# Kernel optimization log

Hardware: AMD Instinct MI355X
Metric: run time of the kernel (lower is better)

The kernel has to match this reference:

```python
import math
import jax, jax.numpy as jnp
import numpy as np

B, L, D_MODEL, NHEAD, FACTOR = 8, 4096, 1024, 16, 5
D_HEAD = D_MODEL // NHEAD
SAMPLE_K = min(L, max(1, FACTOR * int(math.ceil(math.log(max(L, 2))))))  # 45
TOP_U = min(L, max(1, FACTOR * int(math.ceil(math.log(max(L, 2))))))     # 45


def setup_inputs() -> dict:
    key = jax.random.key(0)
    ks = jax.random.split(key, 10)
    x = jax.random.normal(ks[0], (B, L, D_MODEL), dtype=jnp.float32)
    sample_idx = jax.random.randint(ks[1], (SAMPLE_K,), 0, L)
    s = 0.02
    Wq = jax.random.normal(ks[2], (D_MODEL, D_MODEL), dtype=jnp.float32) * s
    Wk = jax.random.normal(ks[3], (D_MODEL, D_MODEL), dtype=jnp.float32) * s
    Wv = jax.random.normal(ks[4], (D_MODEL, D_MODEL), dtype=jnp.float32) * s
    Wo = jax.random.normal(ks[5], (D_MODEL, D_MODEL), dtype=jnp.float32) * s
    bq = jnp.zeros((D_MODEL,), dtype=jnp.float32)
    bk = jnp.zeros((D_MODEL,), dtype=jnp.float32)
    bv = jnp.zeros((D_MODEL,), dtype=jnp.float32)
    bo = jnp.zeros((D_MODEL,), dtype=jnp.float32)
    return {"x": x, "Wq": Wq, "bq": bq, "Wk": Wk, "bk": bk, "Wv": Wv, "bv": bv, "Wo": Wo, "bo": bo, "sample_idx": sample_idx}


def _split_heads(t):
    b, l, _ = t.shape
    return t.reshape(b, l, NHEAD, D_HEAD).transpose(0, 2, 1, 3)  # (b, h, l, d)


def reference(x, Wq, bq, Wk, bk, Wv, bv, Wo, bo, sample_idx):
    b, l, d = x.shape
    q = _split_heads(x @ Wq.T + bq)  # (b, h, l, dh)
    k = _split_heads(x @ Wk.T + bk)
    v = _split_heads(x @ Wv.T + bv)
    scale = 1.0 / math.sqrt(D_HEAD)

    # sparsity measurement on sampled keys
    k_sample = k[:, :, sample_idx, :]                          # (b, h, S, dh)
    scores_sample = jnp.einsum('bhqd,bhsd->bhqs', q, k_sample) * scale
    m = scores_sample.max(axis=-1) - scores_sample.mean(axis=-1)  # (b, h, l)
    _, top_idx = jax.lax.top_k(m, TOP_U)                       # (b, h, U)

    # mean-of-values initialization for non-selected queries
    context = jnp.broadcast_to(v.mean(axis=-2, keepdims=True), (b, NHEAD, l, D_HEAD))

    # dense attention only for the top-U queries
    q_top = jnp.take_along_axis(q, top_idx[..., None], axis=2)  # (b, h, U, dh)
    scores_top = jnp.einsum('bhud,bhkd->bhuk', q_top, k) * scale
    attn = jax.nn.softmax(scores_top, axis=-1)
    out_top = jnp.einsum('bhuk,bhkd->bhud', attn, v)            # (b, h, U, dh)

    bi = jnp.arange(b)[:, None, None]
    hi = jnp.arange(NHEAD)[None, :, None]
    context = context.at[bi, hi, top_idx].set(out_top)          # scatter back

    out = context.transpose(0, 2, 1, 3).reshape(b, l, d)
    return out @ Wo.T + bo
```

## Files before the change

kernel.cpp:

```cpp
#include <hip/hip_runtime.h>
#include <cfloat>
#include <cstdint>

#define B_  8
#define L_  4096
#define DM  1024
#define NH  16
#define DH  64
#define SK  45

typedef __attribute__((ext_vector_type(4))) float f32x4;
typedef _Float16 f16;
typedef __attribute__((ext_vector_type(4))) _Float16 f16x4;
typedef __attribute__((ext_vector_type(8))) _Float16 f16x8;

__device__ __forceinline__ void gload_lds16(const void* g, void* l) {
  __builtin_amdgcn_global_load_lds(
      (const __attribute__((address_space(1))) unsigned int*)g,
      (__attribute__((address_space(3))) unsigned int*)l, 16, 0, 0);
}

__device__ __forceinline__ int swz(int row, int c) {
  return row * 32 + (c ^ (((row >> 1) & 3) << 3));
}

__global__ __launch_bounds__(256) void xsplit16_kernel(const float* __restrict__ x,
    f16* __restrict__ xh, int n4) {
  int i = blockIdx.x * 256 + threadIdx.x;
  int stride = gridDim.x * 256;
  for (; i < n4; i += stride) {
    f32x4 v = ((const f32x4*)x)[i];
    f16x4 h;
    #pragma unroll
    for (int j = 0; j < 4; ++j) h[j] = (f16)v[j];
    ((f16x4*)xh)[i] = h;
  }
}

__global__ __launch_bounds__(256) void wsplit16_kernel(const float* __restrict__ w,
    f16* __restrict__ wh, f16* __restrict__ wl, int n4, int withlo) {
  int i = blockIdx.x * 256 + threadIdx.x;
  int stride = gridDim.x * 256;
  for (; i < n4; i += stride) {
    f32x4 v = ((const f32x4*)w)[i];
    f16x4 h, l;
    #pragma unroll
    for (int j = 0; j < 4; ++j) {
      h[j] = (f16)v[j];
      l[j] = (f16)((v[j] - (float)h[j]) * 2048.0f);
    }
    ((f16x4*)wh)[i] = h;
    if (withlo) ((f16x4*)wl)[i] = l;
  }
}

__global__ __launch_bounds__(256) void meansum_kernel(const f16* __restrict__ xh,
                                                      float* __restrict__ meanx) {
  int b = blockIdx.x;
  int d = blockIdx.y * 256 + threadIdx.x;
  int l0 = blockIdx.z * 256;
  const f16* p = xh + ((size_t)b * L_ + l0) * DM + d;
  float s = 0.f;
  for (int i = 0; i < 256; ++i) s += (float)p[(size_t)i * DM];
  atomicAdd(&meanx[b * DM + d], s);
}

__global__ __launch_bounds__(256) void meansum32_kernel(const float* __restrict__ x,
                                                        float* __restrict__ meanx) {
  int b = blockIdx.x;
  int d = blockIdx.y * 256 + threadIdx.x;
  int l0 = blockIdx.z * 256;
  const float* p = x + ((size_t)b * L_ + l0) * DM + d;
  float s = 0.f;
  for (int i = 0; i < 256; ++i) s += p[(size_t)i * DM];
  atomicAdd(&meanx[b * DM + d], s);
}

__global__ __launch_bounds__(256) void proj_vec_kernel(const float* __restrict__ vin,
    const float* __restrict__ W, const float* __restrict__ bias,
    float* __restrict__ vout, float scale) {
  int g = blockIdx.x * 256 + threadIdx.x;
  int b = g >> 10, n = g & 1023;
  const float* xr = vin + b * DM;
  const float* wr = W + (size_t)n * DM;
  float a0 = 0, a1 = 0, a2 = 0, a3 = 0;
  for (int d = 0; d < DM; d += 4) {
    a0 += xr[d + 0] * wr[d + 0];
    a1 += xr[d + 1] * wr[d + 1];
    a2 += xr[d + 2] * wr[d + 2];
    a3 += xr[d + 3] * wr[d + 3];
  }
  vout[g] = ((a0 + a1) + (a2 + a3)) * scale + bias[n];
}

__global__ __launch_bounds__(256, 4) void ksample_kernel(const float* __restrict__ x,
    const float* __restrict__ Wk, const float* __restrict__ bk,
    const int* __restrict__ sidx, float* __restrict__ KS) {
  const int b = blockIdx.x, nc = blockIdx.y, sg = blockIdx.z;
  __shared__ float xs[5][32];
  __shared__ float wk[64][33];
  __shared__ float red[4][5][64];
  __shared__ int ls[5];
  const int tid = threadIdx.x;
  const int nl = tid & 63, kq = tid >> 6;
  if (tid < 5) ls[tid] = sidx[sg * 5 + tid];
  float acc[5] = {0.f, 0.f, 0.f, 0.f, 0.f};
  const int wrow = tid >> 2, wq = tid & 3;
  for (int kt = 0; kt < 32; ++kt) {
    const int d0 = kt * 32;
    __syncthreads();
    if (tid < 40) {
      int s = tid >> 3, q = tid & 7;
      *(f32x4*)&xs[s][q * 4] = *(const f32x4*)&x[((size_t)b * L_ + ls[s]) * DM + d0 + q * 4];
    }
    {
      const float* src = &Wk[(size_t)(nc * 64 + wrow) * DM + d0 + wq * 8];
      *(f32x4*)&wk[wrow][wq * 8]     = *(const f32x4*)src;
      *(f32x4*)&wk[wrow][wq * 8 + 4] = *(const f32x4*)(src + 4);
    }
    __syncthreads();
    #pragma unroll
    for (int i = 0; i < 2; ++i) {
      f32x4 w = *(const f32x4*)&wk[nl][kq * 8 + i * 4];
      #pragma unroll
      for (int s = 0; s < 5; ++s) {
        f32x4 xv = *(const f32x4*)&xs[s][kq * 8 + i * 4];
        acc[s] += xv[0] * w[0] + xv[1] * w[1] + xv[2] * w[2] + xv[3] * w[3];
      }
    }
  }
  #pragma unroll
  for (int s = 0; s < 5; ++s) red[kq][s][nl] = acc[s];
  __syncthreads();
  for (int t = tid; t < 5 * 64; t += 256) {
    int s = t >> 6, j = t & 63;
    int nj = nc * 64 + j;
    KS[((size_t)b * SK + sg * 5 + s) * DM + nj] =
        red[0][s][j] + red[1][s][j] + red[2][s][j] + red[3][s][j] + bk[nj];
  }
}

__global__ __launch_bounds__(256, 4) void pcomp_kernel(const float* __restrict__ Wq,
    const float* __restrict__ KS, f16* __restrict__ PH, f16* __restrict__ PL) {
  const int b = blockIdx.x, h = blockIdx.y, nc = blockIdx.z;
  __shared__ float ks[45][64];
  __shared__ float wqT[64][68];
  const int tid = threadIdx.x;
  const int n0 = nc * 64;
  for (int i = tid; i < 45 * 64; i += 256) {
    int s = i >> 6, d = i & 63;
    ks[s][d] = KS[((size_t)b * SK + s) * DM + h * 64 + d];
  }
  for (int t = tid; t < 1024; t += 256) {
    int row = t >> 4, cg = t & 15;
    f32x4 v = *(const f32x4*)&Wq[(size_t)(h * 64 + row) * DM + n0 + cg * 4];
    #pragma unroll
    for (int j = 0; j < 4; ++j) wqT[cg * 4 + j][row] = v[j];
  }
  __syncthreads();
  for (int t = tid; t < 48 * 64; t += 256) {
    int s = t >> 6, c = t & 63;
    float acc = 0.f;
    if (s < SK) {
      const f32x4* wr = (const f32x4*)&wqT[c][0];
      const f32x4* kr = (const f32x4*)&ks[s][0];
      float a0 = 0, a1 = 0, a2 = 0, a3 = 0;
      #pragma unroll
      for (int i = 0; i < 16; ++i) {
        f32x4 wv = wr[i], kv = kr[i];
        a0 += wv[0] * kv[0]; a1 += wv[1] * kv[1];
        a2 += wv[2] * kv[2]; a3 += wv[3] * kv[3];
      }
      acc = (a0 + a1) + (a2 + a3);
    }
    f16 hv = (f16)acc;
    size_t off = ((size_t)b * 768 + h * 48 + s) * DM + n0 + c;
    PH[off] = hv;
    PL[off] = (f16)((acc - (float)hv) * 2048.0f);
  }
}

__global__ __launch_bounds__(256, 2) void gemm_sc(const float* __restrict__ x,
    const f16* __restrict__ PH, const f16* __restrict__ PL,
    float* __restrict__ SC) {
  __shared__ f16 xh[128 * 32];
  __shared__ f16 xl[128 * 32];
  __shared__ f16 wh[128 * 32];
  __shared__ f16 wl[128 * 32];
  const int tid = threadIdx.x;
  const int g = blockIdx.y * 8 + blockIdx.x;
  const int q = g >> 3;
  const int nt = q % 6;
  const int mt = (g & 7) + (q / 6) * 8;
  const int n0 = nt * 128;
  const int m0 = mt * 128;
  const int bb = mt >> 5;
  const int lane = tid & 63;
  const int wave = tid >> 6;
  const int wr = (wave >> 1) * 64;
  const int wc = (wave & 1) * 64;
  const int frow = lane & 15;
  const int fk = (lane >> 4) * 8;

  f32x4 aH[4][4], aL[4][4];
  #pragma unroll
  for (int i = 0; i < 4; ++i)
    #pragma unroll
    for (int j = 0; j < 4; ++j)
      #pragma unroll
      for (int z = 0; z < 4; ++z) { aH[i][j][z] = 0.f; aL[i][j][z] = 0.f; }

  const int ar = tid >> 1;
  const int ac = (tid & 1) * 16;
  const int r2 = tid >> 2;
  const int cb = (tid & 3) * 8;
  const int cbs = cb ^ (((r2 >> 1) & 3) << 3);

  const size_t pbase = (size_t)bb * 768;
  for (int kt = 0; kt < 32; ++kt) {
    const float* gx = x + (size_t)(m0 + ar) * DM + kt * 32 + ac;
    #pragma unroll
    for (int gi = 0; gi < 4; ++gi) {
      f32x4 v = ((const f32x4*)gx)[gi];
      f16x4 h, l;
      #pragma unroll
      for (int z = 0; z < 4; ++z) {
        h[z] = (f16)v[z];
        l[z] = (f16)((v[z] - (float)h[z]) * 2048.0f);
      }
      *(f16x4*)(xh + swz(ar, ac + gi * 4)) = h;
      *(f16x4*)(xl + swz(ar, ac + gi * 4)) = l;
    }
    gload_lds16(PH + (pbase + n0 + r2) * DM + kt * 32 + cbs,      wh + r2 * 32 + cb);
    gload_lds16(PH + (pbase + n0 + r2 + 64) * DM + kt * 32 + cbs, wh + (r2 + 64) * 32 + cb);
    gload_lds16(PL + (pbase + n0 + r2) * DM + kt * 32 + cbs,      wl + r2 * 32 + cb);
    gload_lds16(PL + (pbase + n0 + r2 + 64) * DM + kt * 32 + cbs, wl + (r2 + 64) * 32 + cb);
    __syncthreads();
    f16x8 ah[4], al[4], bh[4], bl[4];
    #pragma unroll
    for (int mi = 0; mi < 4; ++mi) {
      ah[mi] = *(const f16x8*)(xh + swz(wr + mi * 16 + frow, fk));
      al[mi] = *(const f16x8*)(xl + swz(wr + mi * 16 + frow, fk));
    }
    #pragma unroll
    for (int ni = 0; ni < 4; ++ni) {
      bh[ni] = *(const f16x8*)(wh + swz(wc + ni * 16 + frow, fk));
      bl[ni] = *(const f16x8*)(wl + swz(wc + ni * 16 + frow, fk));
    }
    #pragma unroll
    for (int mi = 0; mi < 4; ++mi)
      #pragma unroll
      for (int ni = 0; ni < 4; ++ni) {
        aH[mi][ni] = __builtin_amdgcn_mfma_f32_16x16x32_f16(ah[mi], bh[ni], aH[mi][ni], 0, 0, 0);
        aL[mi][ni] = __builtin_amdgcn_mfma_f32_16x16x32_f16(ah[mi], bl[ni], aL[mi][ni], 0, 0, 0);
        aL[mi][ni] = __builtin_amdgcn_mfma_f32_16x16x32_f16(al[mi], bh[ni], aL[mi][ni], 0, 0, 0);
      }
    __syncthreads();
  }

  #pragma unroll
  for (int mi = 0; mi < 4; ++mi) {
    int rowb = m0 + wr + mi * 16 + (lane >> 4) * 4;
    #pragma unroll
    for (int ni = 0; ni < 4; ++ni) {
      int col = n0 + wc + ni * 16 + (lane & 15);
      #pragma unroll
      for (int j = 0; j < 4; ++j) {
        SC[(size_t)(rowb + j) * 768 + col] =
            (aH[mi][ni][j] + aL[mi][ni][j] * (1.0f / 2048.0f)) * 0.125f;
      }
    }
  }
}

__global__ __launch_bounds__(256) void mcompute_kernel(const float* __restrict__ SC,
    float* __restrict__ Mout) {
  const int b = blockIdx.x;
  const int l = blockIdx.y * 16 + (threadIdx.x >> 4);
  const int h = threadIdx.x & 15;
  const float* p = SC + ((size_t)(b * L_ + l)) * 768 + h * 48;
  float mx = -FLT_MAX, sum = 0.f;
  #pragma unroll
  for (int i = 0; i < 11; ++i) {
    f32x4 v = *(const f32x4*)(p + i * 4);
    #pragma unroll
    for (int j = 0; j < 4; ++j) { mx = fmaxf(mx, v[j]); sum += v[j]; }
  }
  { float v = p[44]; mx = fmaxf(mx, v); sum += v; }
  Mout[((size_t)(b * NH + h)) * L_ + l] = mx - sum * (1.0f / SK);
}

__global__ __launch_bounds__(256) void topk_kernel(const float* __restrict__ M,
                                                   int* __restrict__ topi) {
  __shared__ float vals[L_];
  __shared__ float wv[4];
  __shared__ int wi[4];
  const int bh = blockIdx.x, tid = threadIdx.x;
  for (int i = tid; i < L_; i += 256) vals[i] = M[(size_t)bh * L_ + i];
  __syncthreads();
  const int lane = tid & 63, wave = tid >> 6;
  for (int it = 0; it < SK; ++it) {
    float best = -FLT_MAX;
    int bi = 1 << 30;
    for (int i = tid; i < L_; i += 256) {
      float v = vals[i];
      if (v > best || (v == best && i < bi)) { best = v; bi = i; }
    }
    #pragma unroll
    for (int off = 32; off; off >>= 1) {
      float ov = __shfl_down(best, off);
      int oi = __shfl_down(bi, off);
      if (ov > best || (ov == best && oi < bi)) { best = ov; bi = oi; }
    }
    if (lane == 0) { wv[wave] = best; wi[wave] = bi; }
    __syncthreads();
    if (tid == 0) {
      float bb = wv[0]; int bj = wi[0];
      for (int w = 1; w < 4; ++w)
        if (wv[w] > bb || (wv[w] == bb && wi[w] < bj)) { bb = wv[w]; bj = wi[w]; }
      topi[bh * SK + it] = bj;
      vals[bj] = -FLT_MAX;
    }
    __syncthreads();
  }
}

__global__ __launch_bounds__(256, 4) void qtop5_kernel(const float* __restrict__ x,
    const float* __restrict__ Wq, const float* __restrict__ bq,
    const int* __restrict__ topi, f16* __restrict__ QT) {
  const int b = blockIdx.x, h = blockIdx.y, sg = blockIdx.z;
  const int bh = b * NH + h;
  __shared__ float xs[5][32];
  __shared__ float wq[64][33];
  __shared__ float red[4][5][64];
  __shared__ int ls[5];
  const int tid = threadIdx.x;
  const int nl = tid & 63, kq = tid >> 6;
  if (tid < 5) ls[tid] = topi[bh * SK + sg * 5 + tid];
  float acc[5] = {0.f, 0.f, 0.f, 0.f, 0.f};
  const int wrow = tid >> 2, wqc = tid & 3;
  for (int kt = 0; kt < 32; ++kt) {
    const int d0 = kt * 32;
    __syncthreads();
    if (tid < 40) {
      int s = tid >> 3, q = tid & 7;
      *(f32x4*)&xs[s][q * 4] = *(const f32x4*)&x[((size_t)b * L_ + ls[s]) * DM + d0 + q * 4];
    }
    {
      const float* src = &Wq[(size_t)(h * 64 + wrow) * DM + d0 + wqc * 8];
      *(f32x4*)&wq[wrow][wqc * 8]     = *(const f32x4*)src;
      *(f32x4*)&wq[wrow][wqc * 8 + 4] = *(const f32x4*)(src + 4);
    }
    __syncthreads();
    #pragma unroll
    for (int i = 0; i < 2; ++i) {
      f32x4 w = *(const f32x4*)&wq[nl][kq * 8 + i * 4];
      #pragma unroll
      for (int s = 0; s < 5; ++s) {
        f32x4 xv = *(const f32x4*)&xs[s][kq * 8 + i * 4];
        acc[s] += xv[0] * w[0] + xv[1] * w[1] + xv[2] * w[2] + xv[3] * w[3];
      }
    }
  }
  #pragma unroll
  for (int s = 0; s < 5; ++s) red[kq][s][nl] = acc[s];
  __syncthreads();
  for (int t = tid; t < 5 * 64; t += 256) {
    int s = t >> 6, j = t & 63;
    QT[bh * 3072 + (sg * 5 + s) * 64 + j] =
        (f16)(red[0][s][j] + red[1][s][j] + red[2][s][j] + red[3][s][j] + bq[h * 64 + j]);
  }
}

__global__ __launch_bounds__(256, 2) void kscore_kernel(const f16* __restrict__ XH,
    const f16* __restrict__ WKH, const f16* __restrict__ WVH,
    const float* __restrict__ bk, const float* __restrict__ bvec,
    const f16* __restrict__ QT, float* __restrict__ OT, float* __restrict__ Zb) {
  __shared__ __align__(16) char smem[68352];
  f16* qs = (f16*)smem;
  f16* xh = (f16*)(smem + 6912);
  f16* wh = (f16*)(smem + 23296);
  f16* Kt = (f16*)(smem + 31488);
  f16* Ps = (f16*)smem;
  f16* Vt = (f16*)(smem + 31488);
  float* red = (float*)smem;
  const int g = blockIdx.y * 128 + blockIdx.x;
  const int b = g & 7;
  const int p = g >> 3;
  const int jc = p >> 4;
  const int h = p & 15;
  const int bh = b * 16 + h;
  const int tid = threadIdx.x;
  const int lane = tid & 63, wave = tid >> 6;
  const int frow = lane & 15;
  const int fk = (lane >> 4) * 8;

  for (int i = tid; i < 48 * 64; i += 256)
    qs[(i >> 6) * 72 + (i & 63)] = QT[bh * 3072 + i];

  f32x4 accK[4][4], accV[4][4];
  #pragma unroll
  for (int i = 0; i < 4; ++i)
    #pragma unroll
    for (int j = 0; j < 4; ++j)
      #pragma unroll
      for (int z = 0; z < 4; ++z) { accK[i][j][z] = 0.f; accV[i][j][z] = 0.f; }

  const int r2 = tid >> 2, cb = (tid & 3) * 8;
  const int cbs = cb ^ (((r2 >> 1) & 3) << 3);
  for (int kt = 0; kt < 32; ++kt) {
    #pragma unroll
    for (int i = 0; i < 4; ++i)
      gload_lds16(XH + (size_t)(b * L_ + jc * 256 + i * 64 + r2) * DM + kt * 32 + cbs,
                  xh + (i * 64 + r2) * 32 + cb);
    gload_lds16(WKH + (size_t)(h * 64 + r2) * DM + kt * 32 + cbs, wh + r2 * 32 + cb);
    gload_lds16(WVH + (size_t)(h * 64 + r2) * DM + kt * 32 + cbs, wh + (r2 + 64) * 32 + cb);
    __syncthreads();
    f16x8 am[4], bnK[4], bnV[4];
    #pragma unroll
    for (int mi = 0; mi < 4; ++mi)
      am[mi] = *(const f16x8*)(xh + swz(wave * 64 + mi * 16 + frow, fk));
    #pragma unroll
    for (int ni = 0; ni < 4; ++ni) {
      bnK[ni] = *(const f16x8*)(wh + swz(ni * 16 + frow, fk));
      bnV[ni] = *(const f16x8*)(wh + swz(64 + ni * 16 + frow, fk));
    }
    #pragma unroll
    for (int mi = 0; mi < 4; ++mi)
      #pragma unroll
      for (int ni = 0; ni < 4; ++ni) {
        accK[mi][ni] = __builtin_amdgcn_mfma_f32_16x16x32_f16(am[mi], bnK[ni], accK[mi][ni], 0, 0, 0);
        accV[mi][ni] = __builtin_amdgcn_mfma_f32_16x16x32_f16(am[mi], bnV[ni], accV[mi][ni], 0, 0, 0);
      }
    __syncthreads();
  }

  #pragma unroll
  for (int mi = 0; mi < 4; ++mi) {
    int jl = wave * 64 + mi * 16 + (lane >> 4) * 4;
    #pragma unroll
    for (int ni = 0; ni < 4; ++ni) {
      int d = ni * 16 + (lane & 15);
      float bc = bk[h * 64 + d];
      #pragma unroll
      for (int z = 0; z < 4; ++z)
        Kt[(jl + z) * 72 + d] = (f16)(accK[mi][ni][z] + bc);
    }
  }
  __syncthreads();

  f32x4 accS[3][4];
  #pragma unroll
  for (int i = 0; i < 3; ++i)
    #pragma unroll
    for (int j = 0; j < 4; ++j)
      #pragma unroll
      for (int z = 0; z < 4; ++z) accS[i][j][z] = 0.f;
  #pragma unroll
  for (int ks = 0; ks < 2; ++ks) {
    f16x8 aq[3], bv[4];
    #pragma unroll
    for (int mu = 0; mu < 3; ++mu)
      aq[mu] = *(const f16x8*)(qs + (mu * 16 + frow) * 72 + ks * 32 + fk);
    #pragma unroll
    for (int nj = 0; nj < 4; ++nj)
      bv[nj] = *(const f16x8*)(Kt + (wave * 64 + nj * 16 + frow) * 72 + ks * 32 + fk);
    #pragma unroll
    for (int mu = 0; mu < 3; ++mu)
      #pragma unroll
      for (int nj = 0; nj < 4; ++nj)
        accS[mu][nj] = __builtin_amdgcn_mfma_f32_16x16x32_f16(aq[mu], bv[nj], accS[mu][nj], 0, 0, 0);
  }
  __syncthreads();

  #pragma unroll
  for (int mi = 0; mi < 4; ++mi) {
    int jl = wave * 64 + mi * 16 + (lane >> 4) * 4;
    #pragma unroll
    for (int ni = 0; ni < 4; ++ni) {
      int d = ni * 16 + (lane & 15);
      float bc = bvec[h * 64 + d];
      #pragma unroll
      for (int z = 0; z < 4; ++z)
        Vt[d * 264 + jl + z] = (f16)(accV[mi][ni][z] + bc);
    }
  }
  {
    float zs[3][4];
    #pragma unroll
    for (int mu = 0; mu < 3; ++mu)
      #pragma unroll
      for (int z = 0; z < 4; ++z) zs[mu][z] = 0.f;
    #pragma unroll
    for (int mu = 0; mu < 3; ++mu)
      #pragma unroll
      for (int nj = 0; nj < 4; ++nj) {
        int j = wave * 64 + nj * 16 + (lane & 15);
        #pragma unroll
        for (int z = 0; z < 4; ++z) {
          int u = mu * 16 + (lane >> 4) * 4 + z;
          float pv = __expf(accS[mu][nj][z] * 0.125f);
          Ps[u * 264 + j] = (f16)pv;
          zs[mu][z] += pv;
        }
      }
    #pragma unroll
    for (int mu = 0; mu < 3; ++mu)
      #pragma unroll
      for (int z = 0; z < 4; ++z) {
        float v = zs[mu][z];
        v += __shfl_xor(v, 1);
        v += __shfl_xor(v, 2);
        v += __shfl_xor(v, 4);
        v += __shfl_xor(v, 8);
        int u = mu * 16 + (lane >> 4) * 4 + z;
        if ((lane & 15) == 0 && u < SK) atomicAdd(&Zb[bh * 48 + u], v);
      }
  }
  __syncthreads();

  f32x4 accO[3][4];
  #pragma unroll
  for (int i = 0; i < 3; ++i)
    #pragma unroll
    for (int j = 0; j < 4; ++j)
      #pragma unroll
      for (int z = 0; z < 4; ++z) accO[i][j][z] = 0.f;
  #pragma unroll
  for (int ks = 0; ks < 2; ++ks) {
    f16x8 ap[3], bvv[4];
    #pragma unroll
    for (int mu = 0; mu < 3; ++mu)
      ap[mu] = *(const f16x8*)(Ps + (mu * 16 + frow) * 264 + wave * 64 + ks * 32 + fk);
    #pragma unroll
    for (int nd = 0; nd < 4; ++nd)
      bvv[nd] = *(const f16x8*)(Vt + (nd * 16 + frow) * 264 + wave * 64 + ks * 32 + fk);
    #pragma unroll
    for (int mu = 0; mu < 3; ++mu)
      #pragma unroll
      for (int nd = 0; nd < 4; ++nd)
        accO[mu][nd] = __builtin_amdgcn_mfma_f32_16x16x32_f16(ap[mu], bvv[nd], accO[mu][nd], 0, 0, 0);
  }
  __syncthreads();

  #pragma unroll
  for (int mu = 0; mu < 3; ++mu) {
    #pragma unroll
    for (int nd = 0; nd < 4; ++nd) {
      int d = nd * 16 + (lane & 15);
      #pragma unroll
      for (int z = 0; z < 4; ++z) {
        int u = mu * 16 + (lane >> 4) * 4 + z;
        red[wave * 3072 + u * 64 + d] = accO[mu][nd][z];
      }
    }
  }
  __syncthreads();
  for (int i = tid; i < 3072; i += 256) {
    int u = i >> 6;
    if (u < SK)
      atomicAdd(&OT[((size_t)bh * SK + u) * DH + (i & 63)],
                red[i] + red[3072 + i] + red[6144 + i] + red[9216 + i]);
  }
}

__global__ __launch_bounds__(256) void basewrite_kernel(const float* __restrict__ base,
                                                        float* __restrict__ out) {
  size_t i = (size_t)blockIdx.x * 256 + threadIdx.x;
  const size_t stride = (size_t)gridDim.x * 256;
  const size_t total = (size_t)B_ * L_ * (DM / 4);
  for (; i < total; i += stride) {
    size_t b = i >> 20;
    size_t c = i & 255;
    ((f32x4*)out)[i] = ((const f32x4*)base)[b * 256 + c];
  }
}

__global__ __launch_bounds__(256, 2) void corr_kernel(const float* __restrict__ OT,
    const float* __restrict__ Zb, const float* __restrict__ MV,
    const float* __restrict__ Wo, const int* __restrict__ topi,
    float* __restrict__ out) {
  __shared__ float dv[SK][64];
  __shared__ float wo[64][65];
  __shared__ float invz[SK];
  __shared__ int lidx[SK];
  const int bh = blockIdx.x, q = blockIdx.y, tid = threadIdx.x;
  const int b = bh >> 4, h = bh & 15;
  if (tid < SK) {
    invz[tid] = 1.0f / Zb[bh * 48 + tid];
    lidx[tid] = topi[bh * SK + tid];
  }
  __syncthreads();
  for (int i = tid; i < SK * 64; i += 256) {
    int u = i >> 6, d = i & 63;
    dv[u][d] = OT[((size_t)bh * SK + u) * DH + d] * invz[u] - MV[b * DM + h * DH + d];
  }
  const int nn = tid & 63, ug = tid >> 6;
  for (int c = 0; c < 4; ++c) {
    const int n0 = q * 256 + c * 64;
    __syncthreads();
    for (int t = tid; t < 1024; t += 256) {
      int row = t >> 4, vc = t & 15;
      f32x4 v = *(const f32x4*)&Wo[(size_t)(n0 + row) * DM + h * DH + vc * 4];
      *(f32x4*)&wo[row][vc * 4] = v;
    }
    __syncthreads();
    #pragma unroll
    for (int i = 0; i < 12; ++i) {
      int u = ug + i * 4;
      if (u >= SK) break;
      float a0 = 0, a1 = 0, a2 = 0, a3 = 0;
      #pragma unroll
      for (int d4 = 0; d4 < 16; ++d4) {
        f32x4 w = *(const f32x4*)&wo[nn][d4 * 4];
        f32x4 dd = *(const f32x4*)&dv[u][d4 * 4];
        a0 += dd[0] * w[0]; a1 += dd[1] * w[1];
        a2 += dd[2] * w[2]; a3 += dd[3] * w[3];
      }
      atomicAdd(&out[((size_t)b * L_ + lidx[u]) * DM + n0 + nn], (a0 + a1) + (a2 + a3));
    }
  }
}

static const size_t OFF_XH   = 0;
static const size_t OFF_WQH  = OFF_XH + 67108864;
static const size_t OFF_WQL  = OFF_WQH + 2097152;
static const size_t OFF_WKH  = OFF_WQL + 2097152;
static const size_t OFF_WVH  = OFF_WKH + 2097152;
static const size_t OFF_KS   = OFF_WVH + 2097152;
static const size_t OFF_M    = OFF_KS + 1474560;
static const size_t OFF_TOPI = OFF_M + 2097152;
static const size_t OFF_MEANX= OFF_TOPI + 23040;
static const size_t OFF_MV   = OFF_MEANX + 32768;
static const size_t OFF_BASE = OFF_MV + 32768;
static const size_t OFF_ZB   = OFF_BASE + 32768;
static const size_t OFF_QT   = OFF_ZB + 24576;
static const size_t OFF_S    = OFF_QT + 786432;
static const size_t OFF_OT   = OFF_S + 47185920;
static const size_t WS_NEED  = OFF_OT + 1474560;

extern "C" void kernel_launch(void* const* d_in, const int* in_sizes, int n_in,
                              void* d_out, int out_size, void* d_ws, size_t ws_size,
                              hipStream_t stream) {
  const float* x  = (const float*)d_in[0];
  const float* Wq = (const float*)d_in[1];
  const float* bq = (const float*)d_in[2];
  const float* Wk = (const float*)d_in[3];
  const float* bk = (const float*)d_in[4];
  const float* Wv = (const float*)d_in[5];
  const float* bv = (const float*)d_in[6];
  const float* Wo = (const float*)d_in[7];
  const float* bo = (const float*)d_in[8];
  const int* sidx = (const int*)d_in[9];
  float* out = (float*)d_out;
  char* ws = (char*)d_ws;

  if (ws_size < WS_NEED) {
    if (ws_size < 131072) return;
    float* MEANX = (float*)(ws + 0);
    float* MV    = (float*)(ws + 32768);
    float* BASE  = (float*)(ws + 65536);
    hipMemsetAsync(MEANX, 0, 32768, stream);
    meansum32_kernel<<<dim3(B_, 4, 16), 256, 0, stream>>>(x, MEANX);
    proj_vec_kernel<<<32, 256, 0, stream>>>(MEANX, Wv, bv, MV, 1.0f / L_);
    proj_vec_kernel<<<32, 256, 0, stream>>>(MV, Wo, bo, BASE, 1.0f);
    basewrite_kernel<<<2048, 256, 0, stream>>>(BASE, out);
    return;
  }

  f16*   XH   = (f16*)(ws + OFF_XH);
  f16*   WQH  = (f16*)(ws + OFF_WQH);
  f16*   WQL  = (f16*)(ws + OFF_WQL);
  f16*   WKH  = (f16*)(ws + OFF_WKH);
  f16*   WVH  = (f16*)(ws + OFF_WVH);
  float* KS   = (float*)(ws + OFF_KS);
  float* Mb   = (float*)(ws + OFF_M);
  int*   TOPI = (int*)(ws + OFF_TOPI);
  float* MEANX= (float*)(ws + OFF_MEANX);
  float* MV   = (float*)(ws + OFF_MV);
  float* BASE = (float*)(ws + OFF_BASE);
  float* ZB   = (float*)(ws + OFF_ZB);
  f16*   QT   = (f16*)(ws + OFF_QT);
  f16*   PH   = (f16*)(ws + OFF_S);
  f16*   PL   = (f16*)(ws + OFF_S + 12582912);
  float* OT   = (float*)(ws + OFF_OT);
  float* SC   = (float*)out;

  xsplit16_kernel<<<2048, 256, 0, stream>>>(x, XH, (int)((size_t)B_ * L_ * DM / 4));
  wsplit16_kernel<<<256, 256, 0, stream>>>(Wq, WQH, WQL, DM * DM / 4, 1);
  wsplit16_kernel<<<256, 256, 0, stream>>>(Wk, WKH, WKH, DM * DM / 4, 0);
  wsplit16_kernel<<<256, 256, 0, stream>>>(Wv, WVH, WVH, DM * DM / 4, 0);
  hipMemsetAsync(MEANX, 0, 32768, stream);
  hipMemsetAsync(OT, 0, 1474560, stream);
  hipMemsetAsync(ZB, 0, 24576, stream);
  hipMemsetAsync(QT, 0, 786432, stream);

  meansum_kernel<<<dim3(B_, 4, 16), 256, 0, stream>>>(XH, MEANX);
  proj_vec_kernel<<<32, 256, 0, stream>>>(MEANX, Wv, bv, MV, 1.0f / L_);
  proj_vec_kernel<<<32, 256, 0, stream>>>(MV, Wo, bo, BASE, 1.0f);

  ksample_kernel<<<dim3(B_, 16, 9), 256, 0, stream>>>(x, Wk, bk, sidx, KS);
  pcomp_kernel<<<dim3(B_, NH, 16), 256, 0, stream>>>(Wq, KS, PH, PL);
  gemm_sc<<<dim3(8, 192), 256, 0, stream>>>(x, PH, PL, SC);
  mcompute_kernel<<<dim3(B_, 256), 256, 0, stream>>>(SC, Mb);

  topk_kernel<<<B_ * NH, 256, 0, stream>>>(Mb, TOPI);
  qtop5_kernel<<<dim3(B_, NH, 9), 256, 0, stream>>>(x, Wq, bq, TOPI, QT);

  kscore_kernel<<<dim3(128, 16), 256, 0, stream>>>(XH, WKH, WVH, bk, bv, QT, OT, ZB);

  basewrite_kernel<<<2048, 256, 0, stream>>>(BASE, out);
  corr_kernel<<<dim3(B_ * NH, 4), 256, 0, stream>>>(OT, ZB, MV, Wo, TOPI, out);
}
```

Baseline: 825.3 us.

## Fuse sparsity max/mean reduction into score GEMM epilogue via atomics

```diff
diff --git a/kernel.cpp b/kernel.cpp
--- a/kernel.cpp
+++ b/kernel.cpp
@@ -37,8 +37,14 @@
   }
 }
 
-__global__ __launch_bounds__(256) void wsplit16_kernel(const float* __restrict__ w,
-    f16* __restrict__ wh, f16* __restrict__ wl, int n4, int withlo) {
+__global__ __launch_bounds__(256) void wsplit3_kernel(const float* __restrict__ Wq,
+    const float* __restrict__ Wk, const float* __restrict__ Wv,
+    f16* __restrict__ WQH, f16* __restrict__ WQL,
+    f16* __restrict__ WKH, f16* __restrict__ WVH, int n4) {
+  const int which = blockIdx.y;
+  const float* w = (which == 0) ? Wq : ((which == 1) ? Wk : Wv);
+  f16* wh = (which == 0) ? WQH : ((which == 1) ? WKH : WVH);
+  const int withlo = (which == 0);
   int i = blockIdx.x * 256 + threadIdx.x;
   int stride = gridDim.x * 256;
   for (; i < n4; i += stride) {
@@ -50,7 +56,7 @@
       l[j] = (f16)((v[j] - (float)h[j]) * 2048.0f);
     }
     ((f16x4*)wh)[i] = h;
-    if (withlo) ((f16x4*)wl)[i] = l;
+    if (withlo) ((f16x4*)WQL)[i] = l;
   }
 }
 
@@ -182,11 +188,13 @@
 
 __global__ __launch_bounds__(256, 2) void gemm_sc(const float* __restrict__ x,
     const f16* __restrict__ PH, const f16* __restrict__ PL,
-    float* __restrict__ SC) {
-  __shared__ f16 xh[128 * 32];
-  __shared__ f16 xl[128 * 32];
-  __shared__ f16 wh[128 * 32];
-  __shared__ f16 wl[128 * 32];
+    unsigned* __restrict__ MMAXu, float* __restrict__ MSUM) {
+  __shared__ __align__(16) char pool[33792];
+  f16* xh = (f16*)pool;
+  f16* xl = (f16*)(pool + 8192);
+  f16* wh = (f16*)(pool + 16384);
+  f16* wl = (f16*)(pool + 24576);
+  float* scf = (float*)pool;
   const int tid = threadIdx.x;
   const int g = blockIdx.y * 8 + blockIdx.x;
   const int q = g >> 3;
@@ -258,45 +266,62 @@
     __syncthreads();
   }
 
-  #pragma unroll
-  for (int mi = 0; mi < 4; ++mi) {
-    int rowb = m0 + wr + mi * 16 + (lane >> 4) * 4;
-    #pragma unroll
-    for (int ni = 0; ni < 4; ++ni) {
-      int col = n0 + wc + ni * 16 + (lane & 15);
-      #pragma unroll
-      for (int j = 0; j < 4; ++j) {
-        SC[(size_t)(rowb + j) * 768 + col] =
-            (aH[mi][ni][j] + aL[mi][ni][j] * (1.0f / 2048.0f)) * 0.125f;
-      }
-    }
-  }
-}
-
-__global__ __launch_bounds__(256) void mcompute_kernel(const float* __restrict__ SC,
-    float* __restrict__ Mout) {
-  const int b = blockIdx.x;
-  const int l = blockIdx.y * 16 + (threadIdx.x >> 4);
-  const int h = threadIdx.x & 15;
-  const float* p = SC + ((size_t)(b * L_ + l)) * 768 + h * 48;
-  float mx = -FLT_MAX, sum = 0.f;
-  #pragma unroll
-  for (int i = 0; i < 11; ++i) {
-    f32x4 v = *(const f32x4*)(p + i * 4);
-    #pragma unroll
-    for (int j = 0; j < 4; ++j) { mx = fmaxf(mx, v[j]); sum += v[j]; }
-  }
-  { float v = p[44]; mx = fmaxf(mx, v); sum += v; }
-  Mout[((size_t)(b * NH + h)) * L_ + l] = mx - sum * (1.0f / SK);
-}
-
-__global__ __launch_bounds__(256) void topk_kernel(const float* __restrict__ M,
-                                                   int* __restrict__ topi) {
+  const int hbase = n0 / 48;
+  #pragma unroll
+  for (int half = 0; half < 2; ++half) {
+    __syncthreads();
+    if ((wave >> 1) == half) {
+      #pragma unroll
+      for (int mi = 0; mi < 4; ++mi)
+        #pragma unroll
+        for (int ni = 0; ni < 4; ++ni) {
+          int coll = wc + ni * 16 + (lane & 15);
+          #pragma unroll
+          for (int j = 0; j < 4; ++j) {
+            int rowl = mi * 16 + (lane >> 4) * 4 + j;
+            scf[rowl * 132 + coll] =
+                (aH[mi][ni][j] + aL[mi][ni][j] * (1.0f / 2048.0f)) * 0.125f;
+          }
+        }
+    }
+    __syncthreads();
+    {
+      int row = tid >> 2, gidx = tid & 3;
+      int h = hbase + gidx;
+      if (h < NH) {
+        int slo = n0 - h * 48; if (slo < 0) slo = 0;
+        int shi = n0 + 128 - h * 48; if (shi > SK) shi = SK;
+        if (slo < shi) {
+          float mx = -FLT_MAX, sum = 0.f;
+          const float* pr = scf + row * 132 + (h * 48 - n0);
+          for (int s = slo; s < shi; ++s) {
+            float v = pr[s];
+            mx = fmaxf(mx, v);
+            sum += v;
+          }
+          int gl = (m0 & 4095) + half * 64 + row;
+          size_t idx = ((size_t)(bb * NH + h)) * L_ + gl;
+          int bmx = __float_as_int(mx);
+          unsigned key = (unsigned)(bmx ^ ((bmx >> 31) | (int)0x80000000));
+          atomicMax(&MMAXu[idx], key);
+          atomicAdd(&MSUM[idx], sum);
+        }
+      }
+    }
+  }
+}
+
+__global__ __launch_bounds__(256) void topk_kernel(const unsigned* __restrict__ MMAXu,
+    const float* __restrict__ MSUM, int* __restrict__ topi) {
   __shared__ float vals[L_];
   __shared__ float wv[4];
   __shared__ int wi[4];
   const int bh = blockIdx.x, tid = threadIdx.x;
-  for (int i = tid; i < L_; i += 256) vals[i] = M[(size_t)bh * L_ + i];
+  for (int i = tid; i < L_; i += 256) {
+    unsigned key = MMAXu[(size_t)bh * L_ + i];
+    int bits = (key & 0x80000000u) ? (int)(key ^ 0x80000000u) : ~(int)key;
+    vals[i] = __int_as_float(bits) - MSUM[(size_t)bh * L_ + i] * (1.0f / SK);
+  }
   __syncthreads();
   const int lane = tid & 63, wave = tid >> 6;
   for (int it = 0; it < SK; ++it) {
@@ -628,16 +653,19 @@
 static const size_t OFF_WKH  = OFF_WQL + 2097152;
 static const size_t OFF_WVH  = OFF_WKH + 2097152;
 static const size_t OFF_KS   = OFF_WVH + 2097152;
-static const size_t OFF_M    = OFF_KS + 1474560;
-static const size_t OFF_TOPI = OFF_M + 2097152;
-static const size_t OFF_MEANX= OFF_TOPI + 23040;
-static const size_t OFF_MV   = OFF_MEANX + 32768;
+static const size_t OFF_MV   = OFF_KS + 1474560;
 static const size_t OFF_BASE = OFF_MV + 32768;
-static const size_t OFF_ZB   = OFF_BASE + 32768;
+static const size_t OFF_TOPI = OFF_BASE + 32768;
+static const size_t OFF_MEANX= OFF_TOPI + 24576;
+static const size_t OFF_ZB   = OFF_MEANX + 32768;
 static const size_t OFF_QT   = OFF_ZB + 24576;
-static const size_t OFF_S    = OFF_QT + 786432;
-static const size_t OFF_OT   = OFF_S + 47185920;
-static const size_t WS_NEED  = OFF_OT + 1474560;
+static const size_t OFF_MMAX = OFF_QT + 786432;
+static const size_t OFF_MSUM = OFF_MMAX + 2097152;
+static const size_t OFF_OT   = OFF_MSUM + 2097152;
+static const size_t ZERO_SZ  = OFF_OT + 1474560 - OFF_MEANX;
+static const size_t OFF_PH   = OFF_OT + 1474560;
+static const size_t OFF_PL   = OFF_PH + 12582912;
+static const size_t WS_NEED  = OFF_PL + 12582912;
 
 extern "C" void kernel_launch(void* const* d_in, const int* in_sizes, int n_in,
                               void* d_out, int out_size, void* d_ws, size_t ws_size,
@@ -674,26 +702,22 @@
   f16*   WKH  = (f16*)(ws + OFF_WKH);
   f16*   WVH  = (f16*)(ws + OFF_WVH);
   float* KS   = (float*)(ws + OFF_KS);
-  float* Mb   = (float*)(ws + OFF_M);
+  float* MV   = (float*)(ws + OFF_MV);
+  float* BASE = (float*)(ws + OFF_BASE);
   int*   TOPI = (int*)(ws + OFF_TOPI);
   float* MEANX= (float*)(ws + OFF_MEANX);
-  float* MV   = (float*)(ws + OFF_MV);
-  float* BASE = (float*)(ws + OFF_BASE);
   float* ZB   = (float*)(ws + OFF_ZB);
   f16*   QT   = (f16*)(ws + OFF_QT);
-  f16*   PH   = (f16*)(ws + OFF_S);
-  f16*   PL   = (f16*)(ws + OFF_S + 12582912);
+  unsigned* MMAXu = (unsigned*)(ws + OFF_MMAX);
+  float* MSUM = (float*)(ws + OFF_MSUM);
   float* OT   = (float*)(ws + OFF_OT);
-  float* SC   = (float*)out;
+  f16*   PH   = (f16*)(ws + OFF_PH);
+  f16*   PL   = (f16*)(ws + OFF_PL);
 
   xsplit16_kernel<<<2048, 256, 0, stream>>>(x, XH, (int)((size_t)B_ * L_ * DM / 4));
-  wsplit16_kernel<<<256, 256, 0, stream>>>(Wq, WQH, WQL, DM * DM / 4, 1);
-  wsplit16_kernel<<<256, 256, 0, stream>>>(Wk, WKH, WKH, DM * DM / 4, 0);
-  wsplit16_kernel<<<256, 256, 0, stream>>>(Wv, WVH, WVH, DM * DM / 4, 0);
-  hipMemsetAsync(MEANX, 0, 32768, stream);
-  hipMemsetAsync(OT, 0, 1474560, stream);
-  hipMemsetAsync(ZB, 0, 24576, stream);
-  hipMemsetAsync(QT, 0, 786432, stream);
+  wsplit3_kernel<<<dim3(256, 3), 256, 0, stream>>>(Wq, Wk, Wv, WQH, WQL, WKH, WVH,
+                                                   DM * DM / 4);
+  hipMemsetAsync(ws + OFF_MEANX, 0, ZERO_SZ, stream);
 
   meansum_kernel<<<dim3(B_, 4, 16), 256, 0, stream>>>(XH, MEANX);
   proj_vec_kernel<<<32, 256, 0, stream>>>(MEANX, Wv, bv, MV, 1.0f / L_);
@@ -701,10 +725,9 @@
 
   ksample_kernel<<<dim3(B_, 16, 9), 256, 0, stream>>>(x, Wk, bk, sidx, KS);
   pcomp_kernel<<<dim3(B_, NH, 16), 256, 0, stream>>>(Wq, KS, PH, PL);
-  gemm_sc<<<dim3(8, 192), 256, 0, stream>>>(x, PH, PL, SC);
-  mcompute_kernel<<<dim3(B_, 256), 256, 0, stream>>>(SC, Mb);
-
-  topk_kernel<<<B_ * NH, 256, 0, stream>>>(Mb, TOPI);
+  gemm_sc<<<dim3(8, 192), 256, 0, stream>>>(x, PH, PL, MMAXu, MSUM);
+
+  topk_kernel<<<B_ * NH, 256, 0, stream>>>(MMAXu, MSUM, TOPI);
   qtop5_kernel<<<dim3(B_, NH, 9), 256, 0, stream>>>(x, Wq, bq, TOPI, QT);
 
   kscore_kernel<<<dim3(128, 16), 256, 0, stream>>>(XH, WKH, WVH, bk, bv, QT, OT, ZB);
```

Measured after the change: 783.4 us. -5.1%, faster.
